# Kernel tuning notes

Hardware: AMD Instinct MI355X
Metric: run time of the kernel (lower is better)

The kernel has to match this reference:

```python
import jax, jax.numpy as jnp
import numpy as np

CH = 256  # channels

def setup_inputs() -> dict:
    key = jax.random.key(0)
    ks = jax.random.split(key, 9)
    B, H, W = 8, 64, 64
    c8, c2 = CH // 8, CH // 2
    s = lambda fan_in: 1.0 / np.sqrt(fan_in)
    return {
        "x": jax.random.normal(ks[0], (B, H, W, CH), dtype=jnp.float32),
        "Wq": jax.random.normal(ks[1], (CH, c8), dtype=jnp.float32) * s(CH),
        "bq": jnp.zeros((c8,), dtype=jnp.float32),
        "Wk": jax.random.normal(ks[2], (CH, c8), dtype=jnp.float32) * s(CH),
        "bk": jnp.zeros((c8,), dtype=jnp.float32),
        "Wv": jax.random.normal(ks[3], (CH, c2), dtype=jnp.float32) * s(CH),
        "bv": jnp.zeros((c2,), dtype=jnp.float32),
        "Wo": jax.random.normal(ks[4], (c2, CH), dtype=jnp.float32) * s(c2),
        "bo": jnp.zeros((CH,), dtype=jnp.float32),
    }

def reference(x, Wq, bq, Wk, bk, Wv, bv, Wo, bo):
    B, H, W, C = x.shape
    # 1x1 convs are per-pixel matmuls over the channel dim
    q = x @ Wq + bq                      # [B,H,W,C/8]
    k = x @ Wk + bk                      # [B,H,W,C/8]
    v = x @ Wv + bv                      # [B,H,W,C/2]
    N = H * W
    qf = q.reshape(B, N, -1)
    kf = k.reshape(B, N, -1)
    vf = v.reshape(B, N, -1)
    # full self-attention over flattened spatial positions (no scaling, per source)
    scores = jnp.einsum('bnd,bmd->bnm', qf, kf)   # [B,N,N]
    attn = jax.nn.softmax(scores, axis=-1)
    out = jnp.einsum('bnm,bmd->bnd', attn, vf)    # [B,N,C/2]
    out = out.reshape(B, H, W, -1)
    return out @ Wo + bo + x
```

## Files before the change

kernel.cpp:

```cpp
#include <hip/hip_runtime.h>

typedef __attribute__((ext_vector_type(8))) short short8;
typedef __attribute__((ext_vector_type(8))) _Float16 half8;
typedef __attribute__((ext_vector_type(2))) float f32x2;
typedef __attribute__((ext_vector_type(4))) float f32x4;
typedef __attribute__((ext_vector_type(16))) float f32x16;

__device__ __forceinline__ unsigned short f2bf(float f) {
  unsigned int u = __float_as_uint(f);
  u += 0x7fffu + ((u >> 16) & 1u);
  return (unsigned short)(u >> 16);
}
__device__ __forceinline__ float bf2f(unsigned short h) {
  return __uint_as_float(((unsigned int)h) << 16);
}
__device__ __forceinline__ unsigned int cvtpk(float a, float b) {
  unsigned int r;
  asm("v_cvt_pk_bf16_f32 %0, %1, %2" : "=v"(r) : "v"(a), "v"(b));
  return r;
}
__device__ __forceinline__ unsigned short f2h(float f) {
  unsigned int r;
  asm("v_cvt_f16_f32 %0, %1" : "=v"(r) : "v"(f));
  return (unsigned short)r;
}
__device__ __forceinline__ float lo16f(unsigned int u) { return __uint_as_float(u << 16); }
__device__ __forceinline__ float hi16f(unsigned int u) { return __uint_as_float(u & 0xffff0000u); }
__device__ __forceinline__ short8 ld8(const unsigned short* p) {
  return *(const short8*)p;
}
__device__ __forceinline__ half8 ld8h(const unsigned short* p) {
  return *(const half8*)p;
}
__device__ __forceinline__ int swap23(int x) {
  return (x & 0x13) | ((x & 4) << 1) | ((x & 8) >> 1);
}
#define MFMA(a, b, c) __builtin_amdgcn_mfma_f32_16x16x32_bf16((a), (b), (c), 0, 0, 0)
#define MFMA32(a, b, c) __builtin_amdgcn_mfma_f32_32x32x16_bf16((a), (b), (c), 0, 0, 0)
#define MFMA32H(a, b, c) __builtin_amdgcn_mfma_f32_32x32x16_f16((a), (b), (c), 0, 0, 0)
#define LOG2E 1.4426950408889634f

typedef const __attribute__((address_space(1))) unsigned int* gas_u32p;
typedef __attribute__((address_space(3))) unsigned int* las_u32p;

__global__ void prep_weights(const float* __restrict__ Wq, const float* __restrict__ Wk,
                             const float* __restrict__ Wv, const float* __restrict__ Wo,
                             unsigned short* __restrict__ Wth, unsigned short* __restrict__ Wtl,
                             unsigned short* __restrict__ WoT) {
  int idx = blockIdx.x * 256 + threadIdx.x;
  if (idx < 192 * 256) {
    int o = idx >> 8, c = idx & 255;
    float w = (o < 32) ? Wq[c * 32 + o] : (o < 64) ? Wk[c * 32 + (o - 32)] : Wv[c * 128 + (o - 64)];
    unsigned short h = f2bf(w);
    Wth[idx] = h;
    Wtl[idx] = f2bf(w - bf2f(h));
  } else if (idx < 192 * 256 + 256 * 128) {
    int j = idx - 192 * 256;
    int c = j >> 7, d = j & 127;
    WoT[j] = f2bf(Wo[d * 256 + c]);
  }
}

__global__ __launch_bounds__(256) void proj_qkv(
    const float* __restrict__ x,
    const unsigned short* __restrict__ Wth, const unsigned short* __restrict__ Wtl,
    const float* __restrict__ bq, const float* __restrict__ bk, const float* __restrict__ bv,
    unsigned short* __restrict__ qh, unsigned short* __restrict__ KVF) {
  __shared__ unsigned short xsh[32][264];
  __shared__ unsigned short xsl[32][264];
  const int pix0 = blockIdx.x * 32;
  const int b = pix0 >> 12;
  const int nloc0 = pix0 & 4095;
  const int tid = threadIdx.x;

#pragma unroll
  for (int i = 0; i < 8; ++i) {
    int chunk = i * 256 + tid;
    int row = chunk >> 6;
    int c4 = (chunk & 63) * 4;
    float4 v = *(const float4*)(x + (size_t)(pix0 + row) * 256 + c4);
    unsigned int h01 = cvtpk(v.x, v.y), h23 = cvtpk(v.z, v.w);
    unsigned int l01 = cvtpk(v.x - lo16f(h01), v.y - hi16f(h01));
    unsigned int l23 = cvtpk(v.z - lo16f(h23), v.w - hi16f(h23));
    uint2 hp, lp;
    hp.x = h01; hp.y = h23;
    lp.x = l01; lp.y = l23;
    *(uint2*)&xsh[row][c4] = hp;
    *(uint2*)&xsl[row][c4] = lp;
  }
  __syncthreads();

  const int wave = tid >> 6, lane = tid & 63, l = lane & 15, qd = lane >> 4;
  const int nt = nloc0 >> 6;
  const int ktc = (nloc0 >> 5) & 1;
  const int ksbase = (nloc0 >> 4) & 2;
  const int hh = qd >> 1;
  const int eb = 4 * (qd & 1);

#pragma unroll
  for (int si = 0; si < 3; ++si) {
    const int sub = wave + si * 4;
    const int outc0 = sub * 16;
    if (si == 0) {
      const float* bp = (outc0 < 32) ? (bq + outc0) : (bk + outc0 - 32);
      const float4 bb = *(const float4*)(bp + 4 * qd);
      f32x4 acc[2];
      acc[0] = (f32x4){bb.x, bb.y, bb.z, bb.w};
      acc[1] = (f32x4){bb.x, bb.y, bb.z, bb.w};
#pragma unroll
      for (int kc = 0; kc < 8; ++kc) {
        short8 whf = ld8(Wth + (size_t)(outc0 + l) * 256 + kc * 32 + qd * 8);
        short8 wlf = ld8(Wtl + (size_t)(outc0 + l) * 256 + kc * 32 + qd * 8);
#pragma unroll
        for (int m = 0; m < 2; ++m) {
          short8 xhf = ld8(&xsh[m * 16 + l][kc * 32 + qd * 8]);
          short8 xlf = ld8(&xsl[m * 16 + l][kc * 32 + qd * 8]);
          acc[m] = MFMA(wlf, xhf, acc[m]);
          acc[m] = MFMA(whf, xlf, acc[m]);
          acc[m] = MFMA(whf, xhf, acc[m]);
        }
      }
      if (outc0 < 32) {
#pragma unroll
        for (int m = 0; m < 2; ++m) {
          const size_t pixel = (size_t)pix0 + m * 16 + l;
          uint2 st;
          st.x = (unsigned int)f2h(acc[m][0] * LOG2E) |
                 ((unsigned int)f2h(acc[m][1] * LOG2E) << 16);
          st.y = (unsigned int)f2h(acc[m][2] * LOG2E) |
                 ((unsigned int)f2h(acc[m][3] * LOG2E) << 16);
          *(uint2*)(qh + pixel * 32 + outc0 + 4 * qd) = st;
        }
      } else {
        const int step = (outc0 - 32) >> 4;
#pragma unroll
        for (int m = 0; m < 2; ++m) {
          const int lpos = swap23(m * 16 + l);
          const size_t koff = (size_t)(b * 64 + nt) * 10240 +
                              (ktc * 2 + step) * 512 + (hh * 32 + lpos) * 8 + eb;
          uint2 st;
          st.x = (unsigned int)f2h(acc[m][0]) | ((unsigned int)f2h(acc[m][1]) << 16);
          st.y = (unsigned int)f2h(acc[m][2]) | ((unsigned int)f2h(acc[m][3]) << 16);
          *(uint2*)(KVF + koff) = st;
        }
      }
    } else {
      const int dv = (outc0 - 64) + l;
      const float bias = bv[dv];
      f32x4 acc[2];
      acc[0] = (f32x4){bias, bias, bias, bias};
      acc[1] = (f32x4){bias, bias, bias, bias};
#pragma unroll
      for (int kc = 0; kc < 8; ++kc) {
        short8 whf = ld8(Wth + (size_t)(outc0 + l) * 256 + kc * 32 + qd * 8);
#pragma unroll
        for (int m = 0; m < 2; ++m) {
          short8 xhf = ld8(&xsh[m * 16 + l][kc * 32 + qd * 8]);
          acc[m] = MFMA(xhf, whf, acc[m]);
        }
      }
      const int dt = dv >> 5, lam = dv & 31;
#pragma unroll
      for (int m = 0; m < 2; ++m) {
        const int ks = ksbase + m;
        const size_t voff = (size_t)(b * 64 + nt) * 10240 + 2048 +
                            (dt * 4 + ks) * 512 + (hh * 32 + lam) * 8 + eb;
        uint2 st;
        st.x = cvtpk(acc[m][0], acc[m][1]);
        st.y = cvtpk(acc[m][2], acc[m][3]);
        *(uint2*)(KVF + voff) = st;
      }
    }
  }
}

__device__ __forceinline__ void stage_kv(const unsigned short* __restrict__ src,
                                         unsigned short* dst, int wave, int lane) {
#pragma unroll
  for (int i = 0; i < 5; ++i) {
    const int c = wave * 5 + i;
    __builtin_amdgcn_global_load_lds(
        (gas_u32p)(const void*)(src + c * 512 + lane * 8),
        (las_u32p)(void*)(dst + c * 512), 16, 0, 0);
  }
}

__global__ __launch_bounds__(256, 4) void flash_attn(
    const unsigned short* __restrict__ qh,
    const unsigned short* __restrict__ KVF, unsigned short* __restrict__ opart,
    float* __restrict__ lstat) {
  __shared__ unsigned short kv[2][10240];
  const int b = blockIdx.x & 7;
  const int r7 = blockIdx.x >> 3;
  const int tile = r7 & 31;
  const int split = r7 >> 5;
  const int wave = threadIdx.x >> 6;
  const int lane = threadIdx.x & 63;
  const int lam = lane & 31;
  const int h = lane >> 5;
  const int m0 = tile * 128 + wave * 32;
  const int nt0 = split * 16;

  const unsigned short* qh_b = qh + (size_t)b * 4096 * 32;
  const unsigned short* kv_b = KVF + (size_t)b * 64 * 10240;

  half8 qf[2];
#pragma unroll
  for (int step = 0; step < 2; ++step)
    qf[step] = ld8h(qh_b + (size_t)(m0 + lam) * 32 + step * 16 + h * 8);

  f32x16 acc[4];
#pragma unroll
  for (int dt = 0; dt < 4; ++dt)
#pragma unroll
    for (int e = 0; e < 16; ++e) acc[dt][e] = 0.f;
  f32x2 lr = (f32x2){0.f, 0.f};

  stage_kv(kv_b + (size_t)nt0 * 10240, &kv[0][0], wave, lane);
  __syncthreads();

  int cur = 0;
#pragma unroll 1
  for (int it = 0; it < 16; ++it) {
    if (it < 15)
      stage_kv(kv_b + (size_t)(nt0 + it + 1) * 10240, &kv[cur ^ 1][0], wave, lane);

    const unsigned short* cb = &kv[cur][0];

    half8 k0a = ld8h(cb + 0 * 512 + lane * 8);
    half8 k0b = ld8h(cb + 1 * 512 + lane * 8);
    f32x16 z;
#pragma unroll
    for (int e = 0; e < 16; ++e) z[e] = 0.f;
    __builtin_amdgcn_s_setprio(1);
    z = MFMA32H(k0a, qf[0], z);
    z = MFMA32H(k0b, qf[1], z);
    __builtin_amdgcn_s_setprio(0);
    unsigned int ppA[8];
#pragma unroll
    for (int g = 0; g < 8; ++g) {
      float a0 = __builtin_amdgcn_exp2f(z[2 * g]);
      float a1 = __builtin_amdgcn_exp2f(z[2 * g + 1]);
      lr += (f32x2){a0, a1};
      ppA[g] = cvtpk(a0, a1);
    }

    half8 k1a = ld8h(cb + 2 * 512 + lane * 8);
    half8 k1b = ld8h(cb + 3 * 512 + lane * 8);
    f32x16 w;
#pragma unroll
    for (int e = 0; e < 16; ++e) w[e] = 0.f;
    __builtin_amdgcn_s_setprio(1);
    w = MFMA32H(k1a, qf[0], w);
    w = MFMA32H(k1b, qf[1], w);
#pragma unroll
    for (int kss = 0; kss < 2; ++kss) {
      union { unsigned int u[4]; short8 v; } pf;
#pragma unroll
      for (int j = 0; j < 4; ++j) pf.u[j] = ppA[4 * kss + j];
#pragma unroll
      for (int dt = 0; dt < 4; ++dt) {
        short8 vfrag = *(const short8*)(cb + 2048 + (dt * 4 + kss) * 512 + lane * 8);
        acc[dt] = MFMA32(vfrag, pf.v, acc[dt]);
      }
    }
    __builtin_amdgcn_s_setprio(0);
    unsigned int ppB[8];
#pragma unroll
    for (int g = 0; g < 8; ++g) {
      float a0 = __builtin_amdgcn_exp2f(w[2 * g]);
      float a1 = __builtin_amdgcn_exp2f(w[2 * g + 1]);
      lr += (f32x2){a0, a1};
      ppB[g] = cvtpk(a0, a1);
    }
    __builtin_amdgcn_s_setprio(1);
#pragma unroll
    for (int kss = 0; kss < 2; ++kss) {
      union { unsigned int u[4]; short8 v; } pf;
#pragma unroll
      for (int j = 0; j < 4; ++j) pf.u[j] = ppB[4 * kss + j];
#pragma unroll
      for (int dt = 0; dt < 4; ++dt) {
        short8 vfrag = *(const short8*)(cb + 2048 + (dt * 4 + 2 + kss) * 512 + lane * 8);
        acc[dt] = MFMA32(vfrag, pf.v, acc[dt]);
      }
    }
    __builtin_amdgcn_s_setprio(0);

    __syncthreads();
    cur ^= 1;
  }

  const float lrun = lr.x + lr.y;
  const float ltot = lrun + __shfl_xor(lrun, 32);
  const int grow = b * 4096 + m0 + lam;
  if (h == 0) lstat[split * 32768 + grow] = ltot;
  const size_t obase = ((size_t)split * 32768 + grow) * 128;
#pragma unroll
  for (int dt = 0; dt < 4; ++dt)
#pragma unroll
    for (int g = 0; g < 8; ++g) {
      int r = 2 * g;
      int dv = dt * 32 + (r & 3) + 8 * (r >> 2) + 4 * h;
      *(unsigned int*)(opart + obase + dv) = cvtpk(acc[dt][r], acc[dt][r + 1]);
    }
}

__global__ __launch_bounds__(256) void combine_splits(
    const unsigned short* __restrict__ opart, const float* __restrict__ lstat,
    unsigned short* __restrict__ ao) {
  const int tid = threadIdx.x;
  const int row = blockIdx.x * 16 + (tid >> 4);
  const int col = (tid & 15) * 8;
  float den = lstat[row] + lstat[32768 + row] + lstat[65536 + row] + lstat[98304 + row];
  float inv = 1.f / den;
  float o[8] = {0.f, 0.f, 0.f, 0.f, 0.f, 0.f, 0.f, 0.f};
#pragma unroll
  for (int s = 0; s < 4; ++s) {
    uint4 v = *(const uint4*)(opart + ((size_t)s * 32768 + row) * 128 + col);
    unsigned int uu[4] = {v.x, v.y, v.z, v.w};
#pragma unroll
    for (int j = 0; j < 4; ++j) {
      o[2 * j]     += bf2f((unsigned short)(uu[j] & 0xffff));
      o[2 * j + 1] += bf2f((unsigned short)(uu[j] >> 16));
    }
  }
  uint4 outv;
  outv.x = cvtpk(o[0] * inv, o[1] * inv);
  outv.y = cvtpk(o[2] * inv, o[3] * inv);
  outv.z = cvtpk(o[4] * inv, o[5] * inv);
  outv.w = cvtpk(o[6] * inv, o[7] * inv);
  *(uint4*)(ao + (size_t)row * 128 + col) = outv;
}

__global__ __launch_bounds__(256) void out_proj(
    const unsigned short* __restrict__ ao, const unsigned short* __restrict__ WoT,
    const float* __restrict__ bo, const float* __restrict__ x, float* __restrict__ out) {
  const int pix0 = blockIdx.x * 64;
  const int wave = threadIdx.x >> 6, lane = threadIdx.x & 63, l = lane & 15, qd = lane >> 4;
  const int base = pix0 + wave * 16;
  short8 af[4];
#pragma unroll
  for (int kc = 0; kc < 4; ++kc)
    af[kc] = ld8(ao + (size_t)(base + l) * 128 + kc * 32 + qd * 8);
#pragma unroll
  for (int sub = 0; sub < 16; ++sub) {
    const int c0 = sub * 16 + 4 * qd;
    float4 bb = *(const float4*)(bo + c0);
    f32x4 acc = (f32x4){bb.x, bb.y, bb.z, bb.w};
#pragma unroll
    for (int kc = 0; kc < 4; ++kc) {
      short8 wf = ld8(WoT + (size_t)(sub * 16 + l) * 128 + kc * 32 + qd * 8);
      acc = MFMA(wf, af[kc], acc);
    }
    float4 xv = *(const float4*)(x + (size_t)(base + l) * 256 + c0);
    float4 res;
    res.x = acc[0] + xv.x;
    res.y = acc[1] + xv.y;
    res.z = acc[2] + xv.z;
    res.w = acc[3] + xv.w;
    *(float4*)(out + (size_t)(base + l) * 256 + c0) = res;
  }
}

__global__ __launch_bounds__(256) void combine_out(
    const unsigned short* __restrict__ opart, const float* __restrict__ lstat,
    const unsigned short* __restrict__ WoT,
    const float* __restrict__ bo, const float* __restrict__ x, float* __restrict__ out) {
  const int pix0 = blockIdx.x * 64;
  const int wave = threadIdx.x >> 6, lane = threadIdx.x & 63, l = lane & 15, qd = lane >> 4;
  const int base = pix0 + wave * 16;
  const int row = base + l;
  const float den = lstat[row] + lstat[32768 + row] + lstat[65536 + row] + lstat[98304 + row];
  const float inv = 1.f / den;
  short8 af[4];
#pragma unroll
  for (int kc = 0; kc < 4; ++kc) {
    float o[8] = {0.f, 0.f, 0.f, 0.f, 0.f, 0.f, 0.f, 0.f};
#pragma unroll
    for (int s = 0; s < 4; ++s) {
      uint4 v = *(const uint4*)(opart + ((size_t)s * 32768 + row) * 128 + kc * 32 + qd * 8);
      unsigned int uu[4] = {v.x, v.y, v.z, v.w};
#pragma unroll
      for (int j = 0; j < 4; ++j) {
        o[2 * j]     += bf2f((unsigned short)(uu[j] & 0xffff));
        o[2 * j + 1] += bf2f((unsigned short)(uu[j] >> 16));
      }
    }
    union { unsigned int u[4]; short8 v8; } pk;
#pragma unroll
    for (int j = 0; j < 4; ++j) pk.u[j] = cvtpk(o[2 * j] * inv, o[2 * j + 1] * inv);
    af[kc] = pk.v8;
  }
#pragma unroll
  for (int sub = 0; sub < 16; ++sub) {
    const int c0 = sub * 16 + 4 * qd;
    float4 bb = *(const float4*)(bo + c0);
    f32x4 acc = (f32x4){bb.x, bb.y, bb.z, bb.w};
#pragma unroll
    for (int kc = 0; kc < 4; ++kc) {
      short8 wf = ld8(WoT + (size_t)(sub * 16 + l) * 128 + kc * 32 + qd * 8);
      acc = MFMA(wf, af[kc], acc);
    }
    float4 xv = *(const float4*)(x + (size_t)row * 256 + c0);
    float4 res;
    res.x = acc[0] + xv.x;
    res.y = acc[1] + xv.y;
    res.z = acc[2] + xv.z;
    res.w = acc[3] + xv.w;
    *(float4*)(out + (size_t)row * 256 + c0) = res;
  }
}

extern "C" void kernel_launch(void* const* d_in, const int* in_sizes, int n_in,
                              void* d_out, int out_size, void* d_ws, size_t ws_size,
                              hipStream_t stream) {
  const float* x  = (const float*)d_in[0];
  const float* Wq = (const float*)d_in[1];
  const float* bq = (const float*)d_in[2];
  const float* Wk = (const float*)d_in[3];
  const float* bk = (const float*)d_in[4];
  const float* Wv = (const float*)d_in[5];
  const float* bv = (const float*)d_in[6];
  const float* Wo = (const float*)d_in[7];
  const float* bo = (const float*)d_in[8];

  char* ws = (char*)d_ws;
  unsigned short* qh  = (unsigned short*)(ws + 0);
  unsigned short* KVF = (unsigned short*)(ws + 2097152);
  unsigned short* Wth = (unsigned short*)(ws + 12582912);
  unsigned short* Wtl = (unsigned short*)(ws + 12681216);
  unsigned short* WoT = (unsigned short*)(ws + 12779520);
  float*          lst = (float*)(ws + 12845056);
  unsigned short* ao  = (unsigned short*)(ws + 13369344);

  const bool fused = (ws_size >= 50331648ull);
  unsigned short* opart = fused ? (unsigned short*)(ws + 16777216)
                                : (unsigned short*)d_out;

  prep_weights<<<320, 256, 0, stream>>>(Wq, Wk, Wv, Wo, Wth, Wtl, WoT);
  proj_qkv<<<1024, 256, 0, stream>>>(x, Wth, Wtl, bq, bk, bv, qh, KVF);
  flash_attn<<<1024, 256, 0, stream>>>(qh, KVF, opart, lst);
  if (fused) {
    combine_out<<<512, 256, 0, stream>>>(opart, lst, WoT, bo, x, (float*)d_out);
  } else {
    combine_splits<<<2048, 256, 0, stream>>>(opart, lst, ao);
    out_proj<<<512, 256, 0, stream>>>(ao, WoT, bo, x, (float*)d_out);
  }
}
```

Baseline: 189.1 us.

## Halve KV split count in flash attention and prefetch K/V fragments into registers

Cuts the key/value split factor from 4 to 2. Each flash_attn block now walks 32 KV tiles instead of 16, and the grid shrinks from 1024 to 512 blocks. Both combine kernels are updated to sum only two partial outputs and statistics, which lowers partial-output traffic and combine work. All K and V fragments for a tile are now loaded from LDS into registers at the top of each iteration, and launch bounds are relaxed to 2 blocks per SIMD to make room for the extra registers. The risk is lower occupancy and fewer blocks to spread across the CUs.

```diff
diff --git a/kernel.cpp b/kernel.cpp
--- a/kernel.cpp
+++ b/kernel.cpp
@@ -185,7 +185,7 @@
   }
 }
 
-__global__ __launch_bounds__(256, 4) void flash_attn(
+__global__ __launch_bounds__(256, 2) void flash_attn(
     const unsigned short* __restrict__ qh,
     const unsigned short* __restrict__ KVF, unsigned short* __restrict__ opart,
     float* __restrict__ lstat) {
@@ -199,7 +199,7 @@
   const int lam = lane & 31;
   const int h = lane >> 5;
   const int m0 = tile * 128 + wave * 32;
-  const int nt0 = split * 16;
+  const int nt0 = split * 32;
 
   const unsigned short* qh_b = qh + (size_t)b * 4096 * 32;
   const unsigned short* kv_b = KVF + (size_t)b * 64 * 10240;
@@ -221,20 +221,29 @@
 
   int cur = 0;
 #pragma unroll 1
-  for (int it = 0; it < 16; ++it) {
-    if (it < 15)
+  for (int it = 0; it < 32; ++it) {
+    if (it < 31)
       stage_kv(kv_b + (size_t)(nt0 + it + 1) * 10240, &kv[cur ^ 1][0], wave, lane);
 
     const unsigned short* cb = &kv[cur][0];
 
-    half8 k0a = ld8h(cb + 0 * 512 + lane * 8);
-    half8 k0b = ld8h(cb + 1 * 512 + lane * 8);
+    half8 kf[4];
+#pragma unroll
+    for (int j = 0; j < 4; ++j)
+      kf[j] = ld8h(cb + j * 512 + lane * 8);
+    short8 vf[4][4];
+#pragma unroll
+    for (int dt = 0; dt < 4; ++dt)
+#pragma unroll
+      for (int ks = 0; ks < 4; ++ks)
+        vf[dt][ks] = ld8(cb + 2048 + (dt * 4 + ks) * 512 + lane * 8);
+
     f32x16 z;
 #pragma unroll
     for (int e = 0; e < 16; ++e) z[e] = 0.f;
     __builtin_amdgcn_s_setprio(1);
-    z = MFMA32H(k0a, qf[0], z);
-    z = MFMA32H(k0b, qf[1], z);
+    z = MFMA32H(kf[0], qf[0], z);
+    z = MFMA32H(kf[1], qf[1], z);
     __builtin_amdgcn_s_setprio(0);
     unsigned int ppA[8];
 #pragma unroll
@@ -245,24 +254,20 @@
       ppA[g] = cvtpk(a0, a1);
     }
 
-    half8 k1a = ld8h(cb + 2 * 512 + lane * 8);
-    half8 k1b = ld8h(cb + 3 * 512 + lane * 8);
     f32x16 w;
 #pragma unroll
     for (int e = 0; e < 16; ++e) w[e] = 0.f;
     __builtin_amdgcn_s_setprio(1);
-    w = MFMA32H(k1a, qf[0], w);
-    w = MFMA32H(k1b, qf[1], w);
+    w = MFMA32H(kf[2], qf[0], w);
+    w = MFMA32H(kf[3], qf[1], w);
 #pragma unroll
     for (int kss = 0; kss < 2; ++kss) {
       union { unsigned int u[4]; short8 v; } pf;
 #pragma unroll
       for (int j = 0; j < 4; ++j) pf.u[j] = ppA[4 * kss + j];
 #pragma unroll
-      for (int dt = 0; dt < 4; ++dt) {
-        short8 vfrag = *(const short8*)(cb + 2048 + (dt * 4 + kss) * 512 + lane * 8);
-        acc[dt] = MFMA32(vfrag, pf.v, acc[dt]);
-      }
+      for (int dt = 0; dt < 4; ++dt)
+        acc[dt] = MFMA32(vf[dt][kss], pf.v, acc[dt]);
     }
     __builtin_amdgcn_s_setprio(0);
     unsigned int ppB[8];
@@ -280,10 +285,8 @@
 #pragma unroll
       for (int j = 0; j < 4; ++j) pf.u[j] = ppB[4 * kss + j];
 #pragma unroll
-      for (int dt = 0; dt < 4; ++dt) {
-        short8 vfrag = *(const short8*)(cb + 2048 + (dt * 4 + 2 + kss) * 512 + lane * 8);
-        acc[dt] = MFMA32(vfrag, pf.v, acc[dt]);
-      }
+      for (int dt = 0; dt < 4; ++dt)
+        acc[dt] = MFMA32(vf[dt][2 + kss], pf.v, acc[dt]);
     }
     __builtin_amdgcn_s_setprio(0);
 
@@ -312,11 +315,11 @@
   const int tid = threadIdx.x;
   const int row = blockIdx.x * 16 + (tid >> 4);
   const int col = (tid & 15) * 8;
-  float den = lstat[row] + lstat[32768 + row] + lstat[65536 + row] + lstat[98304 + row];
+  float den = lstat[row] + lstat[32768 + row];
   float inv = 1.f / den;
   float o[8] = {0.f, 0.f, 0.f, 0.f, 0.f, 0.f, 0.f, 0.f};
 #pragma unroll
-  for (int s = 0; s < 4; ++s) {
+  for (int s = 0; s < 2; ++s) {
     uint4 v = *(const uint4*)(opart + ((size_t)s * 32768 + row) * 128 + col);
     unsigned int uu[4] = {v.x, v.y, v.z, v.w};
 #pragma unroll
@@ -371,14 +374,14 @@
   const int wave = threadIdx.x >> 6, lane = threadIdx.x & 63, l = lane & 15, qd = lane >> 4;
   const int base = pix0 + wave * 16;
   const int row = base + l;
-  const float den = lstat[row] + lstat[32768 + row] + lstat[65536 + row] + lstat[98304 + row];
+  const float den = lstat[row] + lstat[32768 + row];
   const float inv = 1.f / den;
   short8 af[4];
 #pragma unroll
   for (int kc = 0; kc < 4; ++kc) {
     float o[8] = {0.f, 0.f, 0.f, 0.f, 0.f, 0.f, 0.f, 0.f};
 #pragma unroll
-    for (int s = 0; s < 4; ++s) {
+    for (int s = 0; s < 2; ++s) {
       uint4 v = *(const uint4*)(opart + ((size_t)s * 32768 + row) * 128 + kc * 32 + qd * 8);
       unsigned int uu[4] = {v.x, v.y, v.z, v.w};
 #pragma unroll
@@ -440,7 +443,7 @@
 
   prep_weights<<<320, 256, 0, stream>>>(Wq, Wk, Wv, Wo, Wth, Wtl, WoT);
   proj_qkv<<<1024, 256, 0, stream>>>(x, Wth, Wtl, bq, bk, bv, qh, KVF);
-  flash_attn<<<1024, 256, 0, stream>>>(qh, KVF, opart, lst);
+  flash_attn<<<512, 256, 0, stream>>>(qh, KVF, opart, lst);
   if (fused) {
     combine_out<<<512, 256, 0, stream>>>(opart, lst, WoT, bo, x, (float*)d_out);
   } else {
```

Measured after the change: 182.2 us. -3.7%, faster.
